# Performance work log

Measured on AMD Instinct MI355X. Metric: run time of the kernel, lower is better.

The kernel has to match this reference:

```python
import jax, jax.numpy as jnp
import numpy as np

B, T, D_IN, D_ENC, D_H = 16384, 60, 3, 64, 128


def setup_inputs() -> dict:
    key = jax.random.key(0)
    ks = jax.random.split(key, 10)
    s_enc = 1.0 / np.sqrt(D_IN)
    s_lstm = 1.0 / np.sqrt(D_H)
    s_dec = 1.0 / np.sqrt(D_H)
    return {
        "x": jax.random.normal(ks[0], (B, D_IN), dtype=jnp.float32),
        "W_enc": jax.random.uniform(ks[1], (D_ENC, D_IN), jnp.float32, -s_enc, s_enc),
        "b_enc": jax.random.uniform(ks[2], (D_ENC,), jnp.float32, -s_enc, s_enc),
        "W_ih": jax.random.uniform(ks[3], (4 * D_H, D_ENC), jnp.float32, -s_lstm, s_lstm),
        "W_hh": jax.random.uniform(ks[4], (4 * D_H, D_H), jnp.float32, -s_lstm, s_lstm),
        "b_ih": jax.random.uniform(ks[5], (4 * D_H,), jnp.float32, -s_lstm, s_lstm),
        "b_hh": jax.random.uniform(ks[6], (4 * D_H,), jnp.float32, -s_lstm, s_lstm),
        "W_dec": jax.random.uniform(ks[7], (1, D_H), jnp.float32, -s_dec, s_dec),
        "b_dec": jax.random.uniform(ks[8], (1,), jnp.float32, -s_dec, s_dec),
    }


def _forward(x, W_enc, b_enc, W_ih, W_hh, b_ih, b_hh, W_dec, b_dec):
    encoded = x @ W_enc.T + b_enc  # [B, 64]
    # Input to LSTM is identical at every timestep -> precompute Wx projection once.
    xp = encoded @ W_ih.T + b_ih + b_hh  # [B, 4*H], PyTorch gate order i,f,g,o
    h0 = jnp.zeros((x.shape[0], D_H), x.dtype)
    c0 = jnp.zeros((x.shape[0], D_H), x.dtype)

    def step(carry, _):
        h, c = carry
        gates = xp + h @ W_hh.T  # [B, 4*H]
        i, f, g, o = jnp.split(gates, 4, axis=-1)
        i = jax.nn.sigmoid(i)
        f = jax.nn.sigmoid(f)
        g = jnp.tanh(g)
        o = jax.nn.sigmoid(o)
        c = f * c + i * g
        h = o * jnp.tanh(c)
        return (h, c), h

    (_, _), hs = jax.lax.scan(step, (h0, c0), None, length=T)  # hs: [T, B, H]
    lstm_out = jnp.transpose(hs, (1, 0, 2))  # [B, T, H]
    out = (lstm_out @ W_dec.T + b_dec)[..., 0]  # [B, T]
    return jax.nn.sigmoid(out)


def reference(x, W_enc, b_enc, W_ih, W_hh, b_ih, b_hh, W_dec, b_dec):
    return _forward(x, W_enc, b_enc, W_ih, W_hh, b_ih, b_hh, W_dec, b_dec)
```

## Files before the change

### kernel.cpp

```cpp
#include <hip/hip_runtime.h>

#define T_STEPS 60
#define HID 128
#define ROWS 16
#define NBLK (16384 / ROWS)

typedef __attribute__((ext_vector_type(8))) short short8;
typedef __attribute__((ext_vector_type(4))) float f32x4;

#define K1 1.44269504088896340736f

__device__ __forceinline__ unsigned short f2bf(float f) {
  unsigned u = __float_as_uint(f);
  return (unsigned short)((u + 0x7fffu + ((u >> 16) & 1u)) >> 16);
}
__device__ __forceinline__ float sigm(float x) {
  return __builtin_amdgcn_rcpf(1.0f + __expf(-x));
}

#define HB0 0
#define HB1 4096
#define OUT_BASE 8192
#define LDS_BYTES 12032

__global__ __launch_bounds__(512, 4) void lstm_fused(
    const float* __restrict__ x, const float* __restrict__ W_enc,
    const float* __restrict__ b_enc, const float* __restrict__ W_ih,
    const float* __restrict__ W_hh, const float* __restrict__ b_ih,
    const float* __restrict__ b_hh, const float* __restrict__ W_dec,
    const float* __restrict__ b_dec, float* __restrict__ out) {
  __shared__ __align__(16) unsigned char lds[LDS_BYTES];

  const int tid = threadIdx.x;
  const int wav = tid >> 6;
  const int lane = tid & 63;
  const int l15 = lane & 15;
  const int l4 = lane >> 4;
  const int u = wav * 16 + l15;
  const int row0 = blockIdx.x * ROWS;
  float* outf = (float*)(lds + OUT_BASE);

  for (int i = tid; i < 1024; i += 512) ((unsigned*)(lds + HB0))[i] = 0u;
  for (int i = tid; i < 960; i += 512) outf[i] = 0.0f;

  float xpv[4][4];
  {
    float xr0[4], xr1[4], xr2[4];
#pragma unroll
    for (int v = 0; v < 4; ++v) {
      int r = 4 * l4 + v;
      const float* xp_ = x + (size_t)(row0 + r) * 3;
      xr0[v] = xp_[0];
      xr1[v] = xp_[1];
      xr2[v] = xp_[2];
    }
#pragma unroll
    for (int gt = 0; gt < 4; ++gt) {
      float bias = b_ih[gt * 128 + u] + b_hh[gt * 128 + u];
#pragma unroll
      for (int v = 0; v < 4; ++v) xpv[gt][v] = bias;
    }
    const f32x4* wr0 = (const f32x4*)(W_ih + (size_t)u * 64);
    const f32x4* wr1 = (const f32x4*)(W_ih + (size_t)(128 + u) * 64);
    const f32x4* wr2 = (const f32x4*)(W_ih + (size_t)(256 + u) * 64);
    const f32x4* wr3 = (const f32x4*)(W_ih + (size_t)(384 + u) * 64);
    for (int e4 = 0; e4 < 16; ++e4) {
      f32x4 w0 = wr0[e4], w1 = wr1[e4], w2 = wr2[e4], w3 = wr3[e4];
#pragma unroll
      for (int j = 0; j < 4; ++j) {
        int e = e4 * 4 + j;
        float we0 = W_enc[e * 3], we1 = W_enc[e * 3 + 1], we2 = W_enc[e * 3 + 2];
        float be = b_enc[e];
#pragma unroll
        for (int v = 0; v < 4; ++v) {
          float ev = fmaf(we0, xr0[v], fmaf(we1, xr1[v], fmaf(we2, xr2[v], be)));
          xpv[0][v] = fmaf(w0[j], ev, xpv[0][v]);
          xpv[1][v] = fmaf(w1[j], ev, xpv[1][v]);
          xpv[2][v] = fmaf(w2[j], ev, xpv[2][v]);
          xpv[3][v] = fmaf(w3[j], ev, xpv[3][v]);
        }
      }
    }
#pragma unroll
    for (int gt = 0; gt < 4; ++gt) {
      float s = (gt == 2) ? (-2.0f * K1) : (-K1);
#pragma unroll
      for (int v = 0; v < 4; ++v) xpv[gt][v] *= s;
    }
  }

  short8 bw[4][4];
#pragma unroll
  for (int gt = 0; gt < 4; ++gt) {
    float s = (gt == 2) ? (-2.0f * K1) : (-K1);
#pragma unroll
    for (int kt = 0; kt < 4; ++kt) {
      const float* p = W_hh + (size_t)(gt * 128 + u) * HID + kt * 32 + 8 * l4;
      short8 f;
#pragma unroll
      for (int j = 0; j < 8; ++j) f[j] = (short)f2bf(s * p[j]);
      bw[gt][kt] = f;
    }
  }

  float ct[4];
#pragma unroll
  for (int v = 0; v < 4; ++v) ct[v] = 0.0f;

  const unsigned swzA =
      (((unsigned)(l15 & 7)) << 4) ^ (((unsigned)(l15 & 8)) << 2);
  unsigned rdA[4];
#pragma unroll
  for (int kt = 0; kt < 4; ++kt)
    rdA[kt] = ((unsigned)(l15 * 256 + l4 * 16 + kt * 64)) ^ swzA;
  unsigned wrA[4];
#pragma unroll
  for (int v = 0; v < 4; ++v) {
    unsigned rr = (unsigned)(4 * l4 + v);
    wrA[v] = (rr * 256 + (unsigned)u * 2) ^ ((rr & 7u) << 4) ^ ((rr & 8u) << 2);
  }
  const float wdu = W_dec[u];
  const float kneg = -2.0f * K1;
  const float kpos = 2.0f * K1;

  __syncthreads();

#define STEP(RB, WB, tcur)                                                     \
  {                                                                            \
    f32x4 acc[4];                                                              \
    _Pragma("unroll") for (int gt = 0; gt < 4; ++gt) {                         \
      acc[gt][0] = xpv[gt][0];                                                 \
      acc[gt][1] = xpv[gt][1];                                                 \
      acc[gt][2] = xpv[gt][2];                                                 \
      acc[gt][3] = xpv[gt][3];                                                 \
    }                                                                          \
    _Pragma("unroll") for (int kt = 0; kt < 4; ++kt) {                         \
      short8 af = *(const short8*)(lds + (RB) + rdA[kt]);                      \
      _Pragma("unroll") for (int gt = 0; gt < 4; ++gt) acc[gt] =               \
          __builtin_amdgcn_mfma_f32_16x16x32_bf16(af, bw[gt][kt], acc[gt],     \
                                                  0, 0, 0);                    \
    }                                                                          \
    float pz[4];                                                               \
    _Pragma("unroll") for (int v = 0; v < 4; ++v) {                            \
      float ea = __builtin_amdgcn_exp2f(acc[0][v]);                \
      float ef = __builtin_amdgcn_exp2f(acc[1][v]);                \
      float eg = __builtin_amdgcn_exp2f(acc[2][v]);               \
      float eo = __builtin_amdgcn_exp2f(acc[3][v]);                \
      float A = 1.0f + ea, F = 1.0f + ef, G = 1.0f + eg, Bo = 1.0f + eo;       \
      float AG = A * G;                                                        \
      float r = __builtin_amdgcn_rcpf(F * AG);                                 \
      float t = fmaf(kpos, eg, kneg);                            \
      float num = fmaf(ct[v], AG, t * F);                                      \
      float cn = num * r;                                                      \
      ct[v] = cn;                                                              \
      float ec = __builtin_amdgcn_exp2f(cn);                      \
      float r2 = __builtin_amdgcn_rcpf(Bo * (1.0f + ec));                      \
      float h = (1.0f - ec) * r2;                             \
      *(unsigned short*)(lds + (WB) + wrA[v]) = f2bf(h);                       \
      pz[v] = h * wdu;                                                         \
    }                                                                          \
    _Pragma("unroll") for (int v = 0; v < 4; ++v) {                            \
      pz[v] += __shfl_xor(pz[v], 1, 64);                                       \
      pz[v] += __shfl_xor(pz[v], 2, 64);                                       \
      pz[v] += __shfl_xor(pz[v], 4, 64);                                       \
      pz[v] += __shfl_xor(pz[v], 8, 64);                                       \
    }                                                                          \
    if (l15 == 0) {                                                            \
      _Pragma("unroll") for (int v = 0; v < 4; ++v)                            \
          atomicAdd(&outf[(4 * l4 + v) * T_STEPS + (tcur)], pz[v]);            \
    }                                                                          \
    __syncthreads();                                                           \
  }

  for (int t = 0; t < T_STEPS; t += 2) {
    STEP(HB0, HB1, t)
    STEP(HB1, HB0, t + 1)
  }
#undef STEP

  const float bdec = b_dec[0];
  for (int i = tid; i < 240; i += 512) {
    int r = i / 15, c4 = i - r * 15;
    f32x4 s = *(const f32x4*)&outf[r * T_STEPS + c4 * 4];
    f32x4 o;
#pragma unroll
    for (int k = 0; k < 4; ++k) o[k] = sigm(s[k] + bdec);
    *(f32x4*)(out + (size_t)(row0 + r) * T_STEPS + c4 * 4) = o;
  }
}

extern "C" void kernel_launch(void* const* d_in, const int* in_sizes, int n_in,
                              void* d_out, int out_size, void* d_ws, size_t ws_size,
                              hipStream_t stream) {
  const float* x = (const float*)d_in[0];
  const float* W_enc = (const float*)d_in[1];
  const float* b_enc = (const float*)d_in[2];
  const float* W_ih = (const float*)d_in[3];
  const float* W_hh = (const float*)d_in[4];
  const float* b_ih = (const float*)d_in[5];
  const float* b_hh = (const float*)d_in[6];
  const float* W_dec = (const float*)d_in[7];
  const float* b_dec = (const float*)d_in[8];
  float* out = (float*)d_out;

  dim3 grid(NBLK);
  dim3 block(512);
  lstm_fused<<<grid, block, 0, stream>>>(x, W_enc, b_enc, W_ih, W_hh, b_ih, b_hh,
                                         W_dec, b_dec, out);
}
```

Before: 266.6 us.

## Process 32 rows per block with dual MFMA streams and LDS partial-sum reduction

```diff
diff --git a/kernel.cpp b/kernel.cpp
--- a/kernel.cpp
+++ b/kernel.cpp
@@ -2,7 +2,7 @@
 
 #define T_STEPS 60
 #define HID 128
-#define ROWS 16
+#define ROWS 32
 #define NBLK (16384 / ROWS)
 
 typedef __attribute__((ext_vector_type(8))) short short8;
@@ -19,11 +19,13 @@
 }
 
 #define HB0 0
-#define HB1 4096
-#define OUT_BASE 8192
-#define LDS_BYTES 12032
-
-__global__ __launch_bounds__(512, 4) void lstm_fused(
+#define HB1 8192
+#define PT0 16384
+#define PT1 17408
+#define OUT_BASE 18432
+#define LDS_BYTES 26112
+
+__global__ __launch_bounds__(512, 2) void lstm_fused(
     const float* __restrict__ x, const float* __restrict__ W_enc,
     const float* __restrict__ b_enc, const float* __restrict__ W_ih,
     const float* __restrict__ W_hh, const float* __restrict__ b_ih,
@@ -40,25 +42,24 @@
   const int row0 = blockIdx.x * ROWS;
   float* outf = (float*)(lds + OUT_BASE);
 
-  for (int i = tid; i < 1024; i += 512) ((unsigned*)(lds + HB0))[i] = 0u;
-  for (int i = tid; i < 960; i += 512) outf[i] = 0.0f;
-
-  float xpv[4][4];
+  for (int i = tid; i < 2048; i += 512) ((unsigned*)(lds + HB0))[i] = 0u;
+
+  float xpa[4][4], xpb[4][4];
   {
-    float xr0[4], xr1[4], xr2[4];
+    float xa0[4], xa1[4], xa2[4], xb0[4], xb1[4], xb2[4];
 #pragma unroll
     for (int v = 0; v < 4; ++v) {
       int r = 4 * l4 + v;
-      const float* xp_ = x + (size_t)(row0 + r) * 3;
-      xr0[v] = xp_[0];
-      xr1[v] = xp_[1];
-      xr2[v] = xp_[2];
+      const float* pa = x + (size_t)(row0 + r) * 3;
+      const float* pb = x + (size_t)(row0 + 16 + r) * 3;
+      xa0[v] = pa[0]; xa1[v] = pa[1]; xa2[v] = pa[2];
+      xb0[v] = pb[0]; xb1[v] = pb[1]; xb2[v] = pb[2];
     }
 #pragma unroll
     for (int gt = 0; gt < 4; ++gt) {
       float bias = b_ih[gt * 128 + u] + b_hh[gt * 128 + u];
 #pragma unroll
-      for (int v = 0; v < 4; ++v) xpv[gt][v] = bias;
+      for (int v = 0; v < 4; ++v) { xpa[gt][v] = bias; xpb[gt][v] = bias; }
     }
     const f32x4* wr0 = (const f32x4*)(W_ih + (size_t)u * 64);
     const f32x4* wr1 = (const f32x4*)(W_ih + (size_t)(128 + u) * 64);
@@ -73,11 +74,16 @@
         float be = b_enc[e];
 #pragma unroll
         for (int v = 0; v < 4; ++v) {
-          float ev = fmaf(we0, xr0[v], fmaf(we1, xr1[v], fmaf(we2, xr2[v], be)));
-          xpv[0][v] = fmaf(w0[j], ev, xpv[0][v]);
-          xpv[1][v] = fmaf(w1[j], ev, xpv[1][v]);
-          xpv[2][v] = fmaf(w2[j], ev, xpv[2][v]);
-          xpv[3][v] = fmaf(w3[j], ev, xpv[3][v]);
+          float ea = fmaf(we0, xa0[v], fmaf(we1, xa1[v], fmaf(we2, xa2[v], be)));
+          float eb = fmaf(we0, xb0[v], fmaf(we1, xb1[v], fmaf(we2, xb2[v], be)));
+          xpa[0][v] = fmaf(w0[j], ea, xpa[0][v]);
+          xpa[1][v] = fmaf(w1[j], ea, xpa[1][v]);
+          xpa[2][v] = fmaf(w2[j], ea, xpa[2][v]);
+          xpa[3][v] = fmaf(w3[j], ea, xpa[3][v]);
+          xpb[0][v] = fmaf(w0[j], eb, xpb[0][v]);
+          xpb[1][v] = fmaf(w1[j], eb, xpb[1][v]);
+          xpb[2][v] = fmaf(w2[j], eb, xpb[2][v]);
+          xpb[3][v] = fmaf(w3[j], eb, xpb[3][v]);
         }
       }
     }
@@ -85,7 +91,7 @@
     for (int gt = 0; gt < 4; ++gt) {
       float s = (gt == 2) ? (-2.0f * K1) : (-K1);
 #pragma unroll
-      for (int v = 0; v < 4; ++v) xpv[gt][v] *= s;
+      for (int v = 0; v < 4; ++v) { xpa[gt][v] *= s; xpb[gt][v] *= s; }
     }
   }
 
@@ -103,9 +109,9 @@
     }
   }
 
-  float ct[4];
-#pragma unroll
-  for (int v = 0; v < 4; ++v) ct[v] = 0.0f;
+  float cta[4], ctb[4];
+#pragma unroll
+  for (int v = 0; v < 4; ++v) { cta[v] = 0.0f; ctb[v] = 0.0f; }
 
   const unsigned swzA =
       (((unsigned)(l15 & 7)) << 4) ^ (((unsigned)(l15 & 8)) << 2);
@@ -119,68 +125,103 @@
     unsigned rr = (unsigned)(4 * l4 + v);
     wrA[v] = (rr * 256 + (unsigned)u * 2) ^ ((rr & 7u) << 4) ^ ((rr & 8u) << 2);
   }
+  const unsigned ptW = (unsigned)(wav * 32 + 4 * l4) * 4;
   const float wdu = W_dec[u];
   const float kneg = -2.0f * K1;
   const float kpos = 2.0f * K1;
 
   __syncthreads();
 
-#define STEP(RB, WB, tcur)                                                     \
+#define ACT(ACC, CT, H)                                                        \
   {                                                                            \
-    f32x4 acc[4];                                                              \
+    float ea = __builtin_amdgcn_exp2f(ACC[0][vv]);                             \
+    float ef = __builtin_amdgcn_exp2f(ACC[1][vv]);                             \
+    float eg = __builtin_amdgcn_exp2f(ACC[2][vv]);                             \
+    float eo = __builtin_amdgcn_exp2f(ACC[3][vv]);                             \
+    float A = 1.0f + ea, F = 1.0f + ef, G = 1.0f + eg, Bo = 1.0f + eo;         \
+    float AG = A * G;                                                          \
+    float r = __builtin_amdgcn_rcpf(F * AG);                                   \
+    float tt = fmaf(kpos, eg, kneg);                                           \
+    float num = fmaf(CT[vv], AG, tt * F);                                      \
+    float cn = num * r;                                                        \
+    CT[vv] = cn;                                                               \
+    float ec = __builtin_amdgcn_exp2f(cn);                                     \
+    float r2 = __builtin_amdgcn_rcpf(Bo * (1.0f + ec));                        \
+    H = (1.0f - ec) * r2;                                                      \
+  }
+
+#define STEP(RB, WB, PW, PR, tcur)                                             \
+  {                                                                            \
+      \
+    if ((tcur) > 0 && wav == (((tcur)-1) & 7) && lane < 32) {                  \
+      float s = 0.0f;                                                          \
+      _Pragma("unroll") for (int w = 0; w < 8; ++w)                            \
+          s += *(const float*)(lds + (PR) + (unsigned)(w * 32 + lane) * 4);    \
+      outf[lane * T_STEPS + ((tcur)-1)] = s;                                   \
+    }                                                                          \
+    f32x4 acca[4], accb[4];                                                    \
     _Pragma("unroll") for (int gt = 0; gt < 4; ++gt) {                         \
-      acc[gt][0] = xpv[gt][0];                                                 \
-      acc[gt][1] = xpv[gt][1];                                                 \
-      acc[gt][2] = xpv[gt][2];                                                 \
-      acc[gt][3] = xpv[gt][3];                                                 \
+      _Pragma("unroll") for (int v = 0; v < 4; ++v) {                          \
+        acca[gt][v] = xpa[gt][v];                                              \
+        accb[gt][v] = xpb[gt][v];                                              \
+      }                                                                        \
     }                                                                          \
     _Pragma("unroll") for (int kt = 0; kt < 4; ++kt) {                         \
-      short8 af = *(const short8*)(lds + (RB) + rdA[kt]);                      \
-      _Pragma("unroll") for (int gt = 0; gt < 4; ++gt) acc[gt] =               \
-          __builtin_amdgcn_mfma_f32_16x16x32_bf16(af, bw[gt][kt], acc[gt],     \
-                                                  0, 0, 0);                    \
-    }                                                                          \
-    float pz[4];                                                               \
-    _Pragma("unroll") for (int v = 0; v < 4; ++v) {                            \
-      float ea = __builtin_amdgcn_exp2f(acc[0][v]);                \
-      float ef = __builtin_amdgcn_exp2f(acc[1][v]);                \
-      float eg = __builtin_amdgcn_exp2f(acc[2][v]);               \
-      float eo = __builtin_amdgcn_exp2f(acc[3][v]);                \
-      float A = 1.0f + ea, F = 1.0f + ef, G = 1.0f + eg, Bo = 1.0f + eo;       \
-      float AG = A * G;                                                        \
-      float r = __builtin_amdgcn_rcpf(F * AG);                                 \
-      float t = fmaf(kpos, eg, kneg);                            \
-      float num = fmaf(ct[v], AG, t * F);                                      \
-      float cn = num * r;                                                      \
-      ct[v] = cn;                                                              \
-      float ec = __builtin_amdgcn_exp2f(cn);                      \
-      float r2 = __builtin_amdgcn_rcpf(Bo * (1.0f + ec));                      \
-      float h = (1.0f - ec) * r2;                             \
-      *(unsigned short*)(lds + (WB) + wrA[v]) = f2bf(h);                       \
-      pz[v] = h * wdu;                                                         \
-    }                                                                          \
-    _Pragma("unroll") for (int v = 0; v < 4; ++v) {                            \
-      pz[v] += __shfl_xor(pz[v], 1, 64);                                       \
-      pz[v] += __shfl_xor(pz[v], 2, 64);                                       \
-      pz[v] += __shfl_xor(pz[v], 4, 64);                                       \
-      pz[v] += __shfl_xor(pz[v], 8, 64);                                       \
+      short8 afa = *(const short8*)(lds + (RB) + rdA[kt]);                     \
+      short8 afb = *(const short8*)(lds + (RB) + 4096 + rdA[kt]);              \
+      _Pragma("unroll") for (int gt = 0; gt < 4; ++gt) {                       \
+        acca[gt] = __builtin_amdgcn_mfma_f32_16x16x32_bf16(afa, bw[gt][kt],    \
+                                                           acca[gt], 0, 0, 0); \
+        accb[gt] = __builtin_amdgcn_mfma_f32_16x16x32_bf16(afb, bw[gt][kt],    \
+                                                           accb[gt], 0, 0, 0); \
+      }                                                                        \
+    }                                                                          \
+    f32x4 pza, pzb;                                                            \
+    _Pragma("unroll") for (int vv = 0; vv < 4; ++vv) {                         \
+      float ha, hb;                                                            \
+      ACT(acca, cta, ha)                                                       \
+      ACT(accb, ctb, hb)                                                       \
+      *(unsigned short*)(lds + (WB) + wrA[vv]) = f2bf(ha);                     \
+      *(unsigned short*)(lds + (WB) + 4096 + wrA[vv]) = f2bf(hb);              \
+      pza[vv] = ha * wdu;                                                      \
+      pzb[vv] = hb * wdu;                                                      \
+    }                                                                          \
+    _Pragma("unroll") for (int vv = 0; vv < 4; ++vv) {                         \
+      pza[vv] += __shfl_xor(pza[vv], 1, 64);                                   \
+      pzb[vv] += __shfl_xor(pzb[vv], 1, 64);                                   \
+      pza[vv] += __shfl_xor(pza[vv], 2, 64);                                   \
+      pzb[vv] += __shfl_xor(pzb[vv], 2, 64);                                   \
+      pza[vv] += __shfl_xor(pza[vv], 4, 64);                                   \
+      pzb[vv] += __shfl_xor(pzb[vv], 4, 64);                                   \
+      pza[vv] += __shfl_xor(pza[vv], 8, 64);                                   \
+      pzb[vv] += __shfl_xor(pzb[vv], 8, 64);                                   \
     }                                                                          \
     if (l15 == 0) {                                                            \
-      _Pragma("unroll") for (int v = 0; v < 4; ++v)                            \
-          atomicAdd(&outf[(4 * l4 + v) * T_STEPS + (tcur)], pz[v]);            \
+      *(f32x4*)(lds + (PW) + ptW) = pza;                                       \
+      *(f32x4*)(lds + (PW) + 64 + ptW) = pzb;                                  \
     }                                                                          \
     __syncthreads();                                                           \
   }
 
   for (int t = 0; t < T_STEPS; t += 2) {
-    STEP(HB0, HB1, t)
-    STEP(HB1, HB0, t + 1)
+    STEP(HB0, HB1, PT0, PT1, t)
+    STEP(HB1, HB0, PT1, PT0, t + 1)
   }
 #undef STEP
+#undef ACT
+
+  if (wav == ((T_STEPS - 1) & 7) && lane < 32) {
+    float s = 0.0f;
+#pragma unroll
+    for (int w = 0; w < 8; ++w)
+      s += *(const float*)(lds + PT1 + (unsigned)(w * 32 + lane) * 4);
+    outf[lane * T_STEPS + (T_STEPS - 1)] = s;
+  }
+  __syncthreads();
 
   const float bdec = b_dec[0];
-  for (int i = tid; i < 240; i += 512) {
-    int r = i / 15, c4 = i - r * 15;
+  if (tid < 480) {
+    int r = tid / 15, c4 = tid - r * 15;
     f32x4 s = *(const f32x4*)&outf[r * T_STEPS + c4 * 4];
     f32x4 o;
 #pragma unroll
```

Measured after the change: 267.6 us. Within noise of the previous version (+0.4%).

## Compute decoder projection via MFMA on bf16 h, replacing shuffles and LDS atomics

Applied to the files above, without the earlier changes.

```diff
diff --git a/kernel.cpp b/kernel.cpp
--- a/kernel.cpp
+++ b/kernel.cpp
@@ -23,7 +23,7 @@
 #define OUT_BASE 8192
 #define LDS_BYTES 12032
 
-__global__ __launch_bounds__(512, 4) void lstm_fused(
+__global__ __launch_bounds__(512, 3) void lstm_fused(
     const float* __restrict__ x, const float* __restrict__ W_enc,
     const float* __restrict__ b_enc, const float* __restrict__ W_ih,
     const float* __restrict__ W_hh, const float* __restrict__ b_ih,
@@ -41,9 +41,8 @@
   float* outf = (float*)(lds + OUT_BASE);
 
   for (int i = tid; i < 1024; i += 512) ((unsigned*)(lds + HB0))[i] = 0u;
-  for (int i = tid; i < 960; i += 512) outf[i] = 0.0f;
-
-  float xpv[4][4];
+
+  f32x4 xp4[4];
   {
     float xr0[4], xr1[4], xr2[4];
 #pragma unroll
@@ -58,7 +57,7 @@
     for (int gt = 0; gt < 4; ++gt) {
       float bias = b_ih[gt * 128 + u] + b_hh[gt * 128 + u];
 #pragma unroll
-      for (int v = 0; v < 4; ++v) xpv[gt][v] = bias;
+      for (int v = 0; v < 4; ++v) xp4[gt][v] = bias;
     }
     const f32x4* wr0 = (const f32x4*)(W_ih + (size_t)u * 64);
     const f32x4* wr1 = (const f32x4*)(W_ih + (size_t)(128 + u) * 64);
@@ -74,10 +73,10 @@
 #pragma unroll
         for (int v = 0; v < 4; ++v) {
           float ev = fmaf(we0, xr0[v], fmaf(we1, xr1[v], fmaf(we2, xr2[v], be)));
-          xpv[0][v] = fmaf(w0[j], ev, xpv[0][v]);
-          xpv[1][v] = fmaf(w1[j], ev, xpv[1][v]);
-          xpv[2][v] = fmaf(w2[j], ev, xpv[2][v]);
-          xpv[3][v] = fmaf(w3[j], ev, xpv[3][v]);
+          xp4[0][v] = fmaf(w0[j], ev, xp4[0][v]);
+          xp4[1][v] = fmaf(w1[j], ev, xp4[1][v]);
+          xp4[2][v] = fmaf(w2[j], ev, xp4[2][v]);
+          xp4[3][v] = fmaf(w3[j], ev, xp4[3][v]);
         }
       }
     }
@@ -85,7 +84,7 @@
     for (int gt = 0; gt < 4; ++gt) {
       float s = (gt == 2) ? (-2.0f * K1) : (-K1);
 #pragma unroll
-      for (int v = 0; v < 4; ++v) xpv[gt][v] *= s;
+      for (int v = 0; v < 4; ++v) xp4[gt][v] *= s;
     }
   }
 
@@ -103,6 +102,18 @@
     }
   }
 
+  short8 dw[4];
+#pragma unroll
+  for (int kt = 0; kt < 4; ++kt) {
+    short8 f = {};
+    if (l15 == 0) {
+      const float* p = W_dec + kt * 32 + 8 * l4;
+#pragma unroll
+      for (int j = 0; j < 8; ++j) f[j] = (short)f2bf(p[j]);
+    }
+    dw[kt] = f;
+  }
+
   float ct[4];
 #pragma unroll
   for (int v = 0; v < 4; ++v) ct[v] = 0.0f;
@@ -119,68 +130,77 @@
     unsigned rr = (unsigned)(4 * l4 + v);
     wrA[v] = (rr * 256 + (unsigned)u * 2) ^ ((rr & 7u) << 4) ^ ((rr & 8u) << 2);
   }
-  const float wdu = W_dec[u];
   const float kneg = -2.0f * K1;
   const float kpos = 2.0f * K1;
 
   __syncthreads();
 
-#define STEP(RB, WB, tcur)                                                     \
+#define STEP(RB, WB, icur)                                                     \
   {                                                                            \
+    short8 af[4];                                                              \
+    _Pragma("unroll") for (int kt = 0; kt < 4; ++kt) af[kt] =                  \
+        *(const short8*)(lds + (RB) + rdA[kt]);                                \
     f32x4 acc[4];                                                              \
     _Pragma("unroll") for (int gt = 0; gt < 4; ++gt) {                         \
-      acc[gt][0] = xpv[gt][0];                                                 \
-      acc[gt][1] = xpv[gt][1];                                                 \
-      acc[gt][2] = xpv[gt][2];                                                 \
-      acc[gt][3] = xpv[gt][3];                                                 \
+      acc[gt] = __builtin_amdgcn_mfma_f32_16x16x32_bf16(af[0], bw[gt][0],      \
+                                                        xp4[gt], 0, 0, 0);     \
+      _Pragma("unroll") for (int kt = 1; kt < 4; ++kt) acc[gt] =               \
+          __builtin_amdgcn_mfma_f32_16x16x32_bf16(af[kt], bw[gt][kt],          \
+                                                  acc[gt], 0, 0, 0);           \
     }                                                                          \
-    _Pragma("unroll") for (int kt = 0; kt < 4; ++kt) {                         \
-      short8 af = *(const short8*)(lds + (RB) + rdA[kt]);                      \
-      _Pragma("unroll") for (int gt = 0; gt < 4; ++gt) acc[gt] =               \
-          __builtin_amdgcn_mfma_f32_16x16x32_bf16(af, bw[gt][kt], acc[gt],     \
-                                                  0, 0, 0);                    \
-    }                                                                          \
-    float pz[4];                                                               \
+    f32x4 ad = {};                                                             \
+    _Pragma("unroll") for (int kt = 0; kt < 4; ++kt) ad =                      \
+        __builtin_amdgcn_mfma_f32_16x16x32_bf16(af[kt], dw[kt], ad, 0, 0, 0);  \
     _Pragma("unroll") for (int v = 0; v < 4; ++v) {                            \
-      float ea = __builtin_amdgcn_exp2f(acc[0][v]);                \
-      float ef = __builtin_amdgcn_exp2f(acc[1][v]);                \
-      float eg = __builtin_amdgcn_exp2f(acc[2][v]);               \
-      float eo = __builtin_amdgcn_exp2f(acc[3][v]);                \
+      float ea = __builtin_amdgcn_exp2f(acc[0][v]);                            \
+      float ef = __builtin_amdgcn_exp2f(acc[1][v]);                            \
+      float eg = __builtin_amdgcn_exp2f(acc[2][v]);                            \
+      float eo = __builtin_amdgcn_exp2f(acc[3][v]);                            \
       float A = 1.0f + ea, F = 1.0f + ef, G = 1.0f + eg, Bo = 1.0f + eo;       \
       float AG = A * G;                                                        \
       float r = __builtin_amdgcn_rcpf(F * AG);                                 \
-      float t = fmaf(kpos, eg, kneg);                            \
-      float num = fmaf(ct[v], AG, t * F);                                      \
+      float tt = fmaf(kpos, eg, kneg);                                         \
+      float num = fmaf(ct[v], AG, tt * F);                                     \
       float cn = num * r;                                                      \
       ct[v] = cn;                                                              \
-      float ec = __builtin_amdgcn_exp2f(cn);                      \
+      float ec = __builtin_amdgcn_exp2f(cn);                                   \
       float r2 = __builtin_amdgcn_rcpf(Bo * (1.0f + ec));                      \
-      float h = (1.0f - ec) * r2;                             \
+      float h = (1.0f - ec) * r2;                                              \
       *(unsigned short*)(lds + (WB) + wrA[v]) = f2bf(h);                       \
-      pz[v] = h * wdu;                                                         \
     }                                                                          \
-    _Pragma("unroll") for (int v = 0; v < 4; ++v) {                            \
-      pz[v] += __shfl_xor(pz[v], 1, 64);                                       \
-      pz[v] += __shfl_xor(pz[v], 2, 64);                                       \
-      pz[v] += __shfl_xor(pz[v], 4, 64);                                       \
-      pz[v] += __shfl_xor(pz[v], 8, 64);                                       \
-    }                                                                          \
-    if (l15 == 0) {                                                            \
+    if (wav == 0 && l15 == 0 && (icur) > 0) {                                  \
       _Pragma("unroll") for (int v = 0; v < 4; ++v)                            \
-          atomicAdd(&outf[(4 * l4 + v) * T_STEPS + (tcur)], pz[v]);            \
+          outf[(4 * l4 + v) * T_STEPS + (icur)-1] = ad[v];                     \
     }                                                                          \
     __syncthreads();                                                           \
   }
 
-  for (int t = 0; t < T_STEPS; t += 2) {
-    STEP(HB0, HB1, t)
-    STEP(HB1, HB0, t + 1)
+  for (int i = 0; i < T_STEPS; i += 2) {
+    STEP(HB0, HB1, i)
+    STEP(HB1, HB0, i + 1)
   }
 #undef STEP
 
+  if (wav == 0) {
+    short8 af[4];
+#pragma unroll
+    for (int kt = 0; kt < 4; ++kt)
+      af[kt] = *(const short8*)(lds + HB0 + rdA[kt]);
+    f32x4 ad = {};
+#pragma unroll
+    for (int kt = 0; kt < 4; ++kt)
+      ad = __builtin_amdgcn_mfma_f32_16x16x32_bf16(af[kt], dw[kt], ad, 0, 0, 0);
+    if (l15 == 0) {
+#pragma unroll
+      for (int v = 0; v < 4; ++v)
+        outf[(4 * l4 + v) * T_STEPS + (T_STEPS - 1)] = ad[v];
+    }
+  }
+  __syncthreads();
+
   const float bdec = b_dec[0];
-  for (int i = tid; i < 240; i += 512) {
-    int r = i / 15, c4 = i - r * 15;
+  if (tid < 240) {
+    int r = tid / 15, c4 = tid - r * 15;
     f32x4 s = *(const f32x4*)&outf[r * T_STEPS + c4 * 4];
     f32x4 o;
 #pragma unroll
```

After: 287.0 us. 7.7% more time.
